# Kernel tuning notes

Hardware: AMD Instinct MI355X
Metric: run time of the kernel (lower is better)

The kernel has to match this reference:

```python
import jax, jax.numpy as jnp
import numpy as np

# Hyperparameters matching SemiCurrSinkhornKnopp_stable(__init__) with fresh state (u=v=b=None, prior=None)
EPSILON = 0.1
GAMMA = 1.0
RHO = 0.5
STOPERR = 1e-6
NUM_ITERMAX = 50
SEMI_USE = True
STAB_THRESH = 1e8


def setup_inputs() -> dict:
    key = jax.random.key(0)
    logits = jax.random.normal(key, (4, 2048, 512), dtype=jnp.float32)
    return {"logits": logits}


def _sinkhorn_plan(logits):
    B, n, k = logits.shape
    dt = logits.dtype
    # cost = -log softmax(logits); append zero-cost slack column (mu)
    cost = -jax.nn.log_softmax(logits, axis=-1)                     # [B,n,k]
    C = jnp.concatenate([cost, jnp.zeros((B, n, 1), dt)], axis=-1)  # [B,n,k+1]

    Pa = jnp.full((B, n, 1), 1.0 / n, dt)
    Pb = jnp.full((B, k + 1, 1), RHO / k, dt).at[:, -1, :].set(1.0 - RHO)
    fi = GAMMA / (GAMMA + EPSILON)
    tiny = jnp.finfo(dt).eps

    u0 = jnp.zeros((B, n, 1), dt)
    v0 = jnp.zeros((B, k + 1, 1), dt)
    w0 = jnp.ones((B, k, 1), dt)          # w = exp(v[:-1]*(fi-1)/eps) with v=0
    b0 = jnp.full((B, k + 1, 1), 1.0 / (k + 1), dt)
    a0 = jnp.zeros((B, n, 1), dt)
    state0 = (u0, v0, w0, b0, b0, a0, jnp.asarray(1.0, dt), jnp.asarray(False))

    def step(state, _):
        u, v, w, b, last_b, a_prev, err, stabled = state
        active = err > STOPERR  # emulate the data-dependent while-loop
        # Q is a pure function of (u, v): exp((u - C + v^T)/eps); with u=v=0 this is exp(-C/eps)
        Q = jnp.exp((u - C + jnp.swapaxes(v, 1, 2)) / EPSILON)      # [B,n,k+1]
        a = Pa / jnp.matmul(Q, b)                                    # [B,n,1]
        bn = Pb / jnp.matmul(jnp.swapaxes(Q, 1, 2), a)               # [B,k+1,1]
        if SEMI_USE:
            bn = jnp.concatenate(
                [jnp.power(jnp.maximum(bn[:, :-1], tiny), fi) * w, bn[:, -1:]], axis=1)
        err_n = jnp.linalg.norm(bn - last_b)
        # log-domain absorption when scalings blow up
        stab = jnp.maximum(a.max(), bn.max()) > STAB_THRESH
        u_n = jnp.where(stab, u + EPSILON * jnp.log(a), u)
        v_n = jnp.where(stab, v + EPSILON * jnp.log(bn + tiny), v)
        w_n = jnp.where(stab, w * jnp.power(jnp.maximum(bn[:, :-1], tiny), fi - 1.0), w)
        b_n = jnp.where(stab, jnp.ones_like(bn), bn)
        sel = lambda new, old: jnp.where(active, new, old)
        return (sel(u_n, u), sel(v_n, v), sel(w_n, w), sel(b_n, b),
                sel(b_n, last_b), sel(a, a_prev), sel(err_n, err),
                jnp.where(active, stab, stabled)), None

    (u, v, w, b, last_b, a, err, stabled), _ = jax.lax.scan(step, state0, None, length=NUM_ITERMAX)
    Q = jnp.exp((u - C + jnp.swapaxes(v, 1, 2)) / EPSILON)
    # plan = Q if the last iteration absorbed (b reset to ones), else a*Q*b^T; final scaling by n
    plan = jnp.where(stabled, Q, a * Q * jnp.swapaxes(b, 1, 2)) * n
    return plan[:, :, :-1].astype(jnp.float32)  # drop slack column


@jax.jit
def reference(logits):
    return _sinkhorn_plan(logits)
```

## Files before the change

### kernel.cpp

```cpp
#include <hip/hip_runtime.h>
#include <math.h>


#define NWG   256
#define NTHR  512
#define NW    8
#define NROW  2048
#define KC    512
#define KP1   513
#define RPW   32
#define REP   4
#define PARF  8208
#define EPSI  0.1f
#define IEPS  10.0f
#define FI    0.90909090909090906f
#define FIM1  (-0.09090909090909094f)
#define TINY  1.1920928955078125e-07f
#define PA    (1.0f/2048.0f)
#define PBR   (0.5f/512.0f)
#define PBS   0.5f
#define STABT 1.0e8f
#define STOPE 1.0e-6f
#define ITMAX 50

#define AST(p, v)  __hip_atomic_store((p), (v), __ATOMIC_RELAXED, __HIP_MEMORY_SCOPE_AGENT)
#define ALD(p)     __hip_atomic_load((p), __ATOMIC_RELAXED, __HIP_MEMORY_SCOPE_AGENT)
#define AADD(p, v) __hip_atomic_fetch_add((p), (v), __ATOMIC_RELAXED, __HIP_MEMORY_SCOPE_AGENT)

#define WS_ZERO 4416

#define TOT_OUT    4194304
#define SCR_FLOATS (3 * PARF)
#define SCR_OFF    (TOT_OUT - SCR_FLOATS)

__device__ __forceinline__ float wsum(float v) {
#pragma unroll
  for (int m = 32; m > 0; m >>= 1) v += __shfl_xor(v, m, 64);
  return v;
}
__device__ __forceinline__ float wmaxf(float v) {
#pragma unroll
  for (int m = 32; m > 0; m >>= 1) v = fmaxf(v, __shfl_xor(v, m, 64));
  return v;
}

__global__ __launch_bounds__(NTHR)
void sinkhorn_kernel(const float* __restrict__ logits, float* __restrict__ out,
                     unsigned char* __restrict__ ws, float* __restrict__ scr) {
  const int tid  = threadIdx.x;
  const int wg   = blockIdx.x;
  const int lane = tid & 63;
  const int wid  = tid >> 6;
  const int bat  = wg >> 6;
  const int slab = wg & 63;
  const int rep  = slab & (REP - 1);
  const int grp  = wg & 7;

  unsigned*           arrive = (unsigned*)(ws);
  unsigned long long* cons   = (unsigned long long*)(ws + 256);
  float*              amaxa  = (float*)(ws + 2304);
  unsigned*           done   = (unsigned*)(ws + 4352);
  float*              colsum = scr;

  __shared__ float Klds[RPW][KP1];
  __shared__ float ev[KP1], vv[KP1], bb[KP1], bnL[KP1], ww[KC];
  __shared__ float u_s[RPW], kap[RPW], a_s[RPW], alp[RPW];
  __shared__ float wred[NW], redS[NW], redM[NW];
  __shared__ float c_es, c_mx;

  for (int j = tid; j < KP1; j += NTHR) { vv[j] = 0.f; bb[j] = 1.f / 513.f; bnL[j] = 1.f / 513.f; }
  for (int j = tid; j < KC; j += NTHR) ww[j] = 1.f;
  if (tid < RPW) { u_s[tid] = 0.f; kap[tid] = 1.f; a_s[tid] = 0.f; alp[tid] = 0.f; }

  const size_t rowg0 = (size_t)bat * NROW + (size_t)slab * RPW;
  for (int r = wid; r < RPW; r += NW) {
    const float* lp = logits + (rowg0 + (size_t)r) * KC;
    float x[8];
    float mx = -INFINITY;
#pragma unroll
    for (int m = 0; m < 8; ++m) { x[m] = lp[lane + (m << 6)]; mx = fmaxf(mx, x[m]); }
    mx = wmaxf(mx);
    float sm = 0.f;
#pragma unroll
    for (int m = 0; m < 8; ++m) sm += expf(x[m] - mx);
    sm = wsum(sm);
    float lse = mx + logf(sm);
#pragma unroll
    for (int m = 0; m < 8; ++m) Klds[r][lane + (m << 6)] = expf((x[m] - lse) * IEPS);
    if (lane == 0) Klds[r][KC] = 1.f;
  }
  __syncthreads();

  float err_state = 1.f;
  int   stabled = 0;
  int   p = 0;

  for (int t = 0; t < ITMAX; ++t) {
    if (!(err_state > STOPE)) break;
    const int p2 = t & 1;

    for (int j = tid; j < KP1; j += NTHR) ev[j] = __expf(vv[j] * IEPS) * bb[j];
    __syncthreads();

    float wamax = 0.f;
    for (int r = wid; r < RPW; r += NW) {
      float s = 0.f;
#pragma unroll
      for (int m = 0; m < 8; ++m) { int j = lane + (m << 6); s += Klds[r][j] * ev[j]; }
      if (lane == 0) s += Klds[r][KC] * ev[KC];
      s = wsum(s);
      if (lane == 0) {
        float av = PA / (kap[r] * s);
        a_s[r] = av; alp[r] = kap[r] * av;
        wamax = fmaxf(wamax, av);
      }
    }
    if (lane == 0) wred[wid] = wamax;
    __syncthreads();
    if (tid == 0) {
      float m0 = wred[0];
#pragma unroll
      for (int i = 1; i < NW; ++i) m0 = fmaxf(m0, wred[i]);
      AST(&amaxa[p2 * NWG + wg], m0);
    }

    const int pn = (p == 2) ? 0 : (p + 1);
    if (tid < 32) AST(&colsum[pn * PARF + wg * 32 + tid], 0.f);
    if (wg == 0 && tid >= 32 && tid < 48) AST(&colsum[pn * PARF + 8192 + (tid - 32)], 0.f);

    for (int j = tid; j < KP1; j += NTHR) {
      float acc = 0.f;
#pragma unroll
      for (int r = 0; r < RPW; ++r) acc += Klds[r][j] * alp[r];
      (void)AADD(&colsum[p * PARF + (bat * REP + rep) * KP1 + j], acc);
    }

    asm volatile("s_waitcnt vmcnt(0)" ::: "memory");
    __syncthreads();
    if (tid == 0) {
      (void)AADD(&arrive[bat * 16], 1u);
      while (ALD(&arrive[bat * 16]) < 64u * (unsigned)(t + 1)) __builtin_amdgcn_s_sleep(2);
    }
    __syncthreads();

    const float* cb0 = &colsum[p * PARF + bat * REP * KP1];
    float bn0, bn1 = 0.f, esq_c, mx_c;
    {
      const int j = tid;
      float tot = ALD(&cb0[j]) + ALD(&cb0[KP1 + j]) + ALD(&cb0[2 * KP1 + j]) + ALD(&cb0[3 * KP1 + j]);
      float c = __expf(vv[j] * IEPS) * tot;
      float bnr = ((j < KC) ? PBR : PBS) / c;
      bn0 = (j < KC) ? __powf(fmaxf(bnr, TINY), FI) * ww[j] : bnr;
      float d = bn0 - bnL[j];
      esq_c = d * d; mx_c = bn0;
    }
    if (tid == 0) {
      const int j = KC;
      float tot = ALD(&cb0[j]) + ALD(&cb0[KP1 + j]) + ALD(&cb0[2 * KP1 + j]) + ALD(&cb0[3 * KP1 + j]);
      float c = __expf(vv[j] * IEPS) * tot;
      bn1 = PBS / c;
      float d = bn1 - bnL[j];
      esq_c += d * d; mx_c = fmaxf(mx_c, bn1);
    }

    if (slab == 0) {
      float am = (tid < 64) ? ALD(&amaxa[p2 * NWG + bat * 64 + tid]) : 0.f;
      mx_c = fmaxf(mx_c, am);
      float es = wsum(esq_c);
      float mx = wmaxf(mx_c);
      if (lane == 0) { redS[wid] = es; redM[wid] = mx; }
      __syncthreads();
      if (tid == 0) {
        float est = 0.f, mxt = 0.f;
#pragma unroll
        for (int i = 0; i < NW; ++i) { est += redS[i]; mxt = fmaxf(mxt, redM[i]); }
        unsigned long long seq = (unsigned long long)(unsigned)(t + 1) << 32;
        unsigned long long e64 = seq | (unsigned long long)__float_as_uint(est);
        unsigned long long m64 = seq | (unsigned long long)__float_as_uint(mxt);
#pragma unroll
        for (int g = 0; g < 8; ++g) {
          AST(&cons[(size_t)(bat * 8 + g) * 8 + 0], e64);
          AST(&cons[(size_t)(bat * 8 + g) * 8 + 1], m64);
        }
      }
    }

    if (tid == 0) {
      const unsigned seq = (unsigned)(t + 1);
      float est = 0.f, mxt = 0.f;
#pragma unroll
      for (int b = 0; b < 4; ++b) {
        unsigned long long e, m;
        for (;;) { e = ALD(&cons[(size_t)(b * 8 + grp) * 8 + 0]);
                   if ((unsigned)(e >> 32) == seq) break; __builtin_amdgcn_s_sleep(1); }
        for (;;) { m = ALD(&cons[(size_t)(b * 8 + grp) * 8 + 1]);
                   if ((unsigned)(m >> 32) == seq) break; __builtin_amdgcn_s_sleep(1); }
        est += __uint_as_float((unsigned)e);
        mxt = fmaxf(mxt, __uint_as_float((unsigned)m));
      }
      c_es = est; c_mx = mxt;
    }
    __syncthreads();
    const float esq_t = c_es;
    const int stab = (c_mx > STABT) ? 1 : 0;

    {
      const int j = tid;
      if (stab) {
        vv[j] += EPSI * __logf(bn0 + TINY);
        if (j < KC) ww[j] *= __powf(fmaxf(bn0, TINY), FIM1);
        bb[j] = 1.f; bnL[j] = 1.f;
      } else { bb[j] = bn0; bnL[j] = bn0; }
    }
    if (tid == 0) {
      const int j = KC;
      if (stab) { vv[j] += EPSI * __logf(bn1 + TINY); bb[j] = 1.f; bnL[j] = 1.f; }
      else      { bb[j] = bn1; bnL[j] = bn1; }
    }
    if (stab && tid < RPW) {
      u_s[tid] += EPSI * __logf(a_s[tid]);
      kap[tid] = __expf(u_s[tid] * IEPS);
    }
    err_state = sqrtf(esq_t);
    stabled = stab;
    __syncthreads();
    p = pn;
  }

  asm volatile("s_waitcnt vmcnt(0)" ::: "memory");
  __syncthreads();
  if (tid == 0) {
    (void)AADD(done, 1u);
    while (ALD(done) < (unsigned)NWG) __builtin_amdgcn_s_sleep(2);
  }
  __syncthreads();

  for (int j = tid; j < KP1; j += NTHR) ev[j] = __expf(vv[j] * IEPS);
  __syncthreads();
  for (int r = wid; r < RPW; r += NW) {
    float* op = out + (rowg0 + (size_t)r) * KC;
    float kr = kap[r], ar = a_s[r];
#pragma unroll
    for (int m = 0; m < 8; ++m) {
      int j = lane + (m << 6);
      float Q = kr * Klds[r][j] * ev[j];
      float val = stabled ? Q : (ar * Q * bb[j]);
      op[j] = val * 2048.0f;
    }
  }
}

extern "C" void kernel_launch(void* const* d_in, const int* in_sizes, int n_in,
                              void* d_out, int out_size, void* d_ws, size_t ws_size,
                              hipStream_t stream) {
  (void)in_sizes; (void)n_in; (void)out_size; (void)ws_size;
  const float* logits = (const float*)d_in[0];
  float* out = (float*)d_out;
  float* scr = out + SCR_OFF;
  (void)hipMemsetAsync(d_ws, 0, WS_ZERO, stream);
  (void)hipMemsetAsync(scr, 0, SCR_FLOATS * sizeof(float), stream);
  sinkhorn_kernel<<<dim3(NWG), dim3(NTHR), 0, stream>>>(
      logits, out, (unsigned char*)d_ws, scr);
}
```

Baseline: 444.3 us.

## Defer convergence consensus to next iteration and use hierarchical arrival barrier

The per-iteration consensus wait on error and stability is moved to the start of the next iteration, with ring-buffered slots, so it overlaps the next matvec instead of adding a second blocking wait each step. The single per-batch arrival counter becomes a two-level leaf/root counter to reduce atomic contention, and the column-sum replicas double from 4 to 8 to spread atomic adds. Stabilisation is applied lazily using the stored b, and kap is updated multiplicatively instead of via log/exp. This adds more complex slot bookkeeping and a final tail wait, and reads more replicas per column.

```diff
diff --git a/kernel.cpp b/kernel.cpp
--- a/kernel.cpp
+++ b/kernel.cpp
@@ -9,8 +9,8 @@
 #define KC    512
 #define KP1   513
 #define RPW   32
-#define REP   4
-#define PARF  8208
+#define REP   8
+#define PARF  (4 * REP * KP1)
 #define EPSI  0.1f
 #define IEPS  10.0f
 #define FI    0.90909090909090906f
@@ -27,7 +27,7 @@
 #define ALD(p)     __hip_atomic_load((p), __ATOMIC_RELAXED, __HIP_MEMORY_SCOPE_AGENT)
 #define AADD(p, v) __hip_atomic_fetch_add((p), (v), __ATOMIC_RELAXED, __HIP_MEMORY_SCOPE_AGENT)
 
-#define WS_ZERO 4416
+#define WS_ZERO 12352
 
 #define TOT_OUT    4194304
 #define SCR_FLOATS (3 * PARF)
@@ -45,8 +45,8 @@
 }
 
 __global__ __launch_bounds__(NTHR)
-void sinkhorn_kernel(const float* __restrict__ logits, float* __restrict__ out,
-                     unsigned char* __restrict__ ws, float* __restrict__ scr) {
+void sinkhorn_kernel(const float* __restrict__ logits, float* out,
+                     unsigned char* ws, float* colsum) {
   const int tid  = threadIdx.x;
   const int wg   = blockIdx.x;
   const int lane = tid & 63;
@@ -56,21 +56,21 @@
   const int rep  = slab & (REP - 1);
   const int grp  = wg & 7;
 
-  unsigned*           arrive = (unsigned*)(ws);
-  unsigned long long* cons   = (unsigned long long*)(ws + 256);
-  float*              amaxa  = (float*)(ws + 2304);
-  unsigned*           done   = (unsigned*)(ws + 4352);
-  float*              colsum = scr;
+  unsigned*           leafA = (unsigned*)(ws);
+  unsigned*           rootA = (unsigned*)(ws + 1024);
+  unsigned long long* cons  = (unsigned long long*)(ws + 2048);
+  float*              amaxa = (float*)(ws + 10240);
+  unsigned*           done  = (unsigned*)(ws + 12288);
 
   __shared__ float Klds[RPW][KP1];
-  __shared__ float ev[KP1], vv[KP1], bb[KP1], bnL[KP1], ww[KC];
-  __shared__ float u_s[RPW], kap[RPW], a_s[RPW], alp[RPW];
+  __shared__ float ev[KP1], vv[KP1], bb[KP1], ww[KC];
+  __shared__ float kap[RPW], a_s[RPW], alp[RPW];
   __shared__ float wred[NW], redS[NW], redM[NW];
   __shared__ float c_es, c_mx;
 
-  for (int j = tid; j < KP1; j += NTHR) { vv[j] = 0.f; bb[j] = 1.f / 513.f; bnL[j] = 1.f / 513.f; }
+  for (int j = tid; j < KP1; j += NTHR) { vv[j] = 0.f; bb[j] = 1.f / 513.f; }
   for (int j = tid; j < KC; j += NTHR) ww[j] = 1.f;
-  if (tid < RPW) { u_s[tid] = 0.f; kap[tid] = 1.f; a_s[tid] = 0.f; alp[tid] = 0.f; }
+  if (tid < RPW) { kap[tid] = 1.f; a_s[tid] = 0.f; alp[tid] = 0.f; }
 
   const size_t rowg0 = (size_t)bat * NROW + (size_t)slab * RPW;
   for (int r = wid; r < RPW; r += NW) {
@@ -91,27 +91,70 @@
   }
   __syncthreads();
 
-  float err_state = 1.f;
-  int   stabled = 0;
-  int   p = 0;
+  int stabled = 0;
+  int p = 0;
+  bool broke = false;
 
   for (int t = 0; t < ITMAX; ++t) {
-    if (!(err_state > STOPE)) break;
     const int p2 = t & 1;
+    const int pn = (p == 2) ? 0 : (p + 1);
+
+    if (t > 0) {
+      if (tid == 0) {
+        const unsigned tag = (unsigned)t;
+        const int slot = t & 3;
+        float est = 0.f, mxt = 0.f;
+#pragma unroll
+        for (int b = 0; b < 4; ++b) {
+          const unsigned long long* ln = &cons[(size_t)((b * 4 + slot) * 8 + grp) * 8];
+          unsigned long long e, m;
+          for (;;) { e = ALD(&ln[0]); if ((unsigned)(e >> 32) == tag) break;
+                     __builtin_amdgcn_s_sleep(1); }
+          for (;;) { m = ALD(&ln[1]); if ((unsigned)(m >> 32) == tag) break;
+                     __builtin_amdgcn_s_sleep(1); }
+          est += __uint_as_float((unsigned)e);
+          mxt = fmaxf(mxt, __uint_as_float((unsigned)m));
+        }
+        c_es = est; c_mx = mxt;
+      }
+      __syncthreads();
+      const int stab_prev = (c_mx > STABT) ? 1 : 0;
+      stabled = stab_prev;
+      if (stab_prev) {
+        const int j = tid;
+        float bj = bb[j];
+        vv[j] += EPSI * __logf(bj + TINY);
+        if (j < KC) ww[j] *= __powf(fmaxf(bj, TINY), FIM1);
+        bb[j] = 1.f;
+        if (tid == 0) {
+          float bs = bb[KC]; vv[KC] += EPSI * __logf(bs + TINY); bb[KC] = 1.f;
+        }
+        if (tid < RPW) kap[tid] *= a_s[tid];
+      }
+      if (!(sqrtf(c_es) > STOPE)) { broke = true; }
+      __syncthreads();
+      if (broke) break;
+    }
 
     for (int j = tid; j < KP1; j += NTHR) ev[j] = __expf(vv[j] * IEPS) * bb[j];
     __syncthreads();
+
+    float evr[8];
+#pragma unroll
+    for (int m = 0; m < 8; ++m) evr[m] = ev[lane + (m << 6)];
+    const float evs = (lane == 0) ? ev[KC] : 0.f;
 
     float wamax = 0.f;
     for (int r = wid; r < RPW; r += NW) {
       float s = 0.f;
 #pragma unroll
-      for (int m = 0; m < 8; ++m) { int j = lane + (m << 6); s += Klds[r][j] * ev[j]; }
-      if (lane == 0) s += Klds[r][KC] * ev[KC];
+      for (int m = 0; m < 8; ++m) s += Klds[r][lane + (m << 6)] * evr[m];
+      if (lane == 0) s += Klds[r][KC] * evs;
       s = wsum(s);
       if (lane == 0) {
         float av = PA / (kap[r] * s);
-        a_s[r] = av; alp[r] = kap[r] * av;
+        a_s[r] = av;
+        alp[r] = kap[r] * av;
         wamax = fmaxf(wamax, av);
       }
     }
@@ -124,22 +167,33 @@
       AST(&amaxa[p2 * NWG + wg], m0);
     }
 
-    const int pn = (p == 2) ? 0 : (p + 1);
-    if (tid < 32) AST(&colsum[pn * PARF + wg * 32 + tid], 0.f);
-    if (wg == 0 && tid >= 32 && tid < 48) AST(&colsum[pn * PARF + 8192 + (tid - 32)], 0.f);
-
-    for (int j = tid; j < KP1; j += NTHR) {
-      float acc = 0.f;
-#pragma unroll
-      for (int r = 0; r < RPW; ++r) acc += Klds[r][j] * alp[r];
-      (void)AADD(&colsum[p * PARF + (bat * REP + rep) * KP1 + j], acc);
+    {
+      float* zb = &colsum[pn * PARF + bat * REP * KP1];
+      if (tid < 64) AST(&zb[slab * 64 + tid], 0.f);
+      if (slab == 0 && tid >= 64 && tid < 72) AST(&zb[4096 + (tid - 64)], 0.f);
+    }
+
+    {
+      float* cb = &colsum[p * PARF + (bat * REP + rep) * KP1];
+      for (int j = tid; j < KP1; j += NTHR) {
+        float acc = 0.f;
+#pragma unroll
+        for (int r = 0; r < RPW; ++r) acc += Klds[r][j] * alp[r];
+        (void)AADD(&cb[j], acc);
+      }
     }
 
     asm volatile("s_waitcnt vmcnt(0)" ::: "memory");
     __syncthreads();
     if (tid == 0) {
-      (void)AADD(&arrive[bat * 16], 1u);
-      while (ALD(&arrive[bat * 16]) < 64u * (unsigned)(t + 1)) __builtin_amdgcn_s_sleep(2);
+      unsigned* lc = &leafA[(bat * 4 + (slab >> 4)) * 16];
+      unsigned p1 = AADD(lc, 1u);
+      if ((p1 & 15u) == 15u) (void)AADD(&rootA[bat * 16], 1u);
+    }
+
+    if (tid == 0) {
+      const unsigned want = 4u * (unsigned)(t + 1);
+      while (ALD(&rootA[bat * 16]) < want) __builtin_amdgcn_s_sleep(1);
     }
     __syncthreads();
 
@@ -147,21 +201,27 @@
     float bn0, bn1 = 0.f, esq_c, mx_c;
     {
       const int j = tid;
-      float tot = ALD(&cb0[j]) + ALD(&cb0[KP1 + j]) + ALD(&cb0[2 * KP1 + j]) + ALD(&cb0[3 * KP1 + j]);
+      float tot = 0.f;
+#pragma unroll
+      for (int i = 0; i < REP; ++i) tot += ALD(&cb0[i * KP1 + j]);
       float c = __expf(vv[j] * IEPS) * tot;
-      float bnr = ((j < KC) ? PBR : PBS) / c;
-      bn0 = (j < KC) ? __powf(fmaxf(bnr, TINY), FI) * ww[j] : bnr;
-      float d = bn0 - bnL[j];
+      bn0 = __powf(fmaxf(PBR / c, TINY), FI) * ww[j];
+      float d = bn0 - bb[j];
       esq_c = d * d; mx_c = bn0;
     }
     if (tid == 0) {
-      const int j = KC;
-      float tot = ALD(&cb0[j]) + ALD(&cb0[KP1 + j]) + ALD(&cb0[2 * KP1 + j]) + ALD(&cb0[3 * KP1 + j]);
-      float c = __expf(vv[j] * IEPS) * tot;
+      float tot = 0.f;
+#pragma unroll
+      for (int i = 0; i < REP; ++i) tot += ALD(&cb0[i * KP1 + KC]);
+      float c = __expf(vv[KC] * IEPS) * tot;
       bn1 = PBS / c;
-      float d = bn1 - bnL[j];
+      float d = bn1 - bb[KC];
       esq_c += d * d; mx_c = fmaxf(mx_c, bn1);
     }
+    __syncthreads();
+    bb[tid] = bn0;
+    if (tid == 0) bb[KC] = bn1;
+    __syncthreads();
 
     if (slab == 0) {
       float am = (tid < 64) ? ALD(&amaxa[p2 * NWG + bat * 64 + tid]) : 0.f;
@@ -174,57 +234,47 @@
         float est = 0.f, mxt = 0.f;
 #pragma unroll
         for (int i = 0; i < NW; ++i) { est += redS[i]; mxt = fmaxf(mxt, redM[i]); }
-        unsigned long long seq = (unsigned long long)(unsigned)(t + 1) << 32;
-        unsigned long long e64 = seq | (unsigned long long)__float_as_uint(est);
-        unsigned long long m64 = seq | (unsigned long long)__float_as_uint(mxt);
+        const unsigned long long tagw = (unsigned long long)(unsigned)(t + 1) << 32;
+        const unsigned long long e64 = tagw | (unsigned long long)__float_as_uint(est);
+        const unsigned long long m64 = tagw | (unsigned long long)__float_as_uint(mxt);
+        const int slot = (t + 1) & 3;
 #pragma unroll
         for (int g = 0; g < 8; ++g) {
-          AST(&cons[(size_t)(bat * 8 + g) * 8 + 0], e64);
-          AST(&cons[(size_t)(bat * 8 + g) * 8 + 1], m64);
+          unsigned long long* ln = &cons[(size_t)((bat * 4 + slot) * 8 + g) * 8];
+          AST(&ln[0], e64);
+          AST(&ln[1], m64);
         }
       }
     }
-
-    if (tid == 0) {
-      const unsigned seq = (unsigned)(t + 1);
-      float est = 0.f, mxt = 0.f;
+    p = pn;
+  }
+
+  if (!broke) {
+    if (tid == 0) {
+      const unsigned tag = (unsigned)ITMAX;
+      const int slot = ITMAX & 3;
+      float mxt = 0.f;
 #pragma unroll
       for (int b = 0; b < 4; ++b) {
-        unsigned long long e, m;
-        for (;;) { e = ALD(&cons[(size_t)(b * 8 + grp) * 8 + 0]);
-                   if ((unsigned)(e >> 32) == seq) break; __builtin_amdgcn_s_sleep(1); }
-        for (;;) { m = ALD(&cons[(size_t)(b * 8 + grp) * 8 + 1]);
-                   if ((unsigned)(m >> 32) == seq) break; __builtin_amdgcn_s_sleep(1); }
-        est += __uint_as_float((unsigned)e);
+        const unsigned long long* ln = &cons[(size_t)((b * 4 + slot) * 8 + grp) * 8];
+        unsigned long long m;
+        for (;;) { m = ALD(&ln[1]); if ((unsigned)(m >> 32) == tag) break;
+                   __builtin_amdgcn_s_sleep(1); }
         mxt = fmaxf(mxt, __uint_as_float((unsigned)m));
       }
-      c_es = est; c_mx = mxt;
-    }
-    __syncthreads();
-    const float esq_t = c_es;
-    const int stab = (c_mx > STABT) ? 1 : 0;
-
-    {
+      c_mx = mxt;
+    }
+    __syncthreads();
+    stabled = (c_mx > STABT) ? 1 : 0;
+    if (stabled) {
       const int j = tid;
-      if (stab) {
-        vv[j] += EPSI * __logf(bn0 + TINY);
-        if (j < KC) ww[j] *= __powf(fmaxf(bn0, TINY), FIM1);
-        bb[j] = 1.f; bnL[j] = 1.f;
-      } else { bb[j] = bn0; bnL[j] = bn0; }
-    }
-    if (tid == 0) {
-      const int j = KC;
-      if (stab) { vv[j] += EPSI * __logf(bn1 + TINY); bb[j] = 1.f; bnL[j] = 1.f; }
-      else      { bb[j] = bn1; bnL[j] = bn1; }
-    }
-    if (stab && tid < RPW) {
-      u_s[tid] += EPSI * __logf(a_s[tid]);
-      kap[tid] = __expf(u_s[tid] * IEPS);
-    }
-    err_state = sqrtf(esq_t);
-    stabled = stab;
-    __syncthreads();
-    p = pn;
+      float bj = bb[j];
+      vv[j] += EPSI * __logf(bj + TINY);
+      bb[j] = 1.f;
+      if (tid == 0) { float bs = bb[KC]; vv[KC] += EPSI * __logf(bs + TINY); bb[KC] = 1.f; }
+      if (tid < RPW) kap[tid] *= a_s[tid];
+      __syncthreads();
+    }
   }
 
   asm volatile("s_waitcnt vmcnt(0)" ::: "memory");
```

Result: slower. 472.0 us (+6.2%).
